# Performance work log

Measured on AMD Instinct MI355X. Metric: run time of the kernel, lower is better.

## Reference

```python
import jax, jax.numpy as jnp
import numpy as np

N_NODES = 100000
N_EDGES = 1600000
D = 128
L = 3


def setup_inputs() -> dict:
    key = jax.random.key(0)
    ks = jax.random.split(key, 5)
    x = jax.random.normal(ks[0], (N_NODES, D), dtype=jnp.float32)
    # Xavier-ish scale for stability through 3 layers
    scale = 1.0 / np.sqrt(D)
    W_self = jax.random.normal(ks[1], (L, D, D), dtype=jnp.float32) * scale
    W_neigh = jax.random.normal(ks[2], (L, D, D), dtype=jnp.float32) * scale
    bias = jnp.zeros((L, D), dtype=jnp.float32)
    src = jax.random.randint(ks[3], (N_EDGES,), 0, N_NODES)
    dst = jax.random.randint(ks[4], (N_EDGES,), 0, N_NODES)
    return {"x": x, "W_self": W_self, "W_neigh": W_neigh, "bias": bias,
            "src": src, "dst": dst}


def reference(x, W_self, W_neigh, bias, src, dst):
    """HomoSAGEEncoder forward (inference mode, dropout = identity).

    Each layer: DGL SAGEConv('mean'):
        h_neigh[v] = mean_{u in in-neighbors(v)} h[u]   (0 if no neighbors)
        h = h @ W_self + h_neigh @ W_neigh + bias
    followed by ReLU.
    """
    N = x.shape[0]
    n_layers = W_self.shape[0]
    # in-degree per destination node (shared across layers)
    deg = jax.ops.segment_sum(jnp.ones_like(dst, dtype=x.dtype), dst,
                              num_segments=N)
    inv_deg = (1.0 / jnp.maximum(deg, 1.0))[:, None]  # [N,1]

    h = x
    for l in range(n_layers):
        msg = h[src]  # [E,D] gather
        h_neigh = jax.ops.segment_sum(msg, dst, num_segments=N) * inv_deg
        h = h @ W_self[l] + h_neigh @ W_neigh[l] + bias[l]
        h = jax.nn.relu(h)
        # dropout is identity at inference; skipped
    return h
```

## Files before the change

kernel.cpp:

```cpp
#include <hip/hip_runtime.h>

typedef __attribute__((ext_vector_type(8))) short short8;
typedef __attribute__((ext_vector_type(4))) float f32x4;

static constexpr int NN = 100000;
static constexpr int NE = 1600000;
static constexpr int DD = 128;
static constexpr int NBUCK = 196;
static constexpr int CAP = 9216;

static constexpr int OFF_GCUR = 0;
static constexpr int OFF_OFFS = 512;
static constexpr int OFF_INV  = 100516;
static constexpr int OFF_WT   = 200520;
static constexpr int OFF_SS   = 249680;
static constexpr int OFF_HB   = 1849680;
static constexpr int OFF_HC   = 8249680;

__device__ inline ushort f2b(float f) {
  uint u = __builtin_bit_cast(uint, f);
  uint r = (u + 0x7fffu + ((u >> 16) & 1u)) >> 16;
  return (ushort)r;
}
__device__ inline float b2f(ushort b) {
  uint u = ((uint)b) << 16;
  return __builtin_bit_cast(float, u);
}

__global__ __launch_bounds__(256) void k_pre(const float* __restrict__ x,
                                             const float* __restrict__ Ws,
                                             const float* __restrict__ Wn,
                                             ushort* __restrict__ hb,
                                             ushort* __restrict__ WtP,
                                             int* __restrict__ gcur) {
  int b = blockIdx.x, t = threadIdx.x;
  if (b < 12500) {
    int i = b * 256 + t;
    float4 v = *(const float4*)(x + (size_t)i * 4);
    uint2 p;
    p.x = (uint)f2b(v.x) | ((uint)f2b(v.y) << 16);
    p.y = (uint)f2b(v.z) | ((uint)f2b(v.w) << 16);
    *(uint2*)(hb + (size_t)i * 4) = p;
  } else if (b < 12884) {
    int i = (b - 12500) * 256 + t;
    int j = i & 7;
    int kg = (i >> 3) & 3;
    int col = (i >> 5) & 127;
    int kt = (i >> 12) & 7;
    int l = i >> 15;
    int k = kt * 32 + kg * 8 + j;
    float v = (k < 128) ? Ws[((size_t)l * 128 + k) * 128 + col]
                        : Wn[((size_t)l * 128 + (k - 128)) * 128 + col];
    WtP[i] = f2b(v);
  } else {
    gcur[t] = 0;
  }
}

__global__ __launch_bounds__(256) void k_bucket(const int* __restrict__ src,
                                                const int* __restrict__ dst,
                                                int* __restrict__ gcur,
                                                int2* __restrict__ ebuf) {
  __shared__ int cnt[NBUCK], base[NBUCK];
  int t = threadIdx.x;
  int b0 = blockIdx.x * 4096;
  if (t < NBUCK) cnt[t] = 0;
  __syncthreads();
  int dv[16], pv[16];
#pragma unroll
  for (int j = 0; j < 16; ++j) {
    int idx = b0 + j * 256 + t;
    if (idx < NE) {
      int d = dst[idx];
      dv[j] = d;
      pv[j] = atomicAdd(&cnt[d >> 9], 1);
    } else dv[j] = -1;
  }
  __syncthreads();
  if (t < NBUCK) base[t] = atomicAdd(&gcur[t], cnt[t]);
  __syncthreads();
#pragma unroll
  for (int j = 0; j < 16; ++j) {
    if (dv[j] >= 0) {
      int idx = b0 + j * 256 + t;
      int b = dv[j] >> 9;
      int2 pr; pr.x = src[idx]; pr.y = dv[j];
      ebuf[(size_t)b * CAP + base[b] + pv[j]] = pr;
    }
  }
}

__global__ __launch_bounds__(256) void k_sort(const int2* __restrict__ ebuf,
                                              const int* __restrict__ gcur,
                                              int* __restrict__ offs,
                                              float* __restrict__ inv,
                                              int* __restrict__ ss) {
  __shared__ int cnt[512];
  __shared__ int sbase[512];
  __shared__ int scan[256];
  __shared__ int sarr[CAP];
  int b = blockIdx.x, t = threadIdx.x;
  int gv = (t < NBUCK) ? gcur[t] : 0;
  scan[t] = gv;
  __syncthreads();
  for (int off = 1; off < 256; off <<= 1) {
    int u = (t >= off) ? scan[t - off] : 0;
    __syncthreads();
    scan[t] += u;
    __syncthreads();
  }
  int nB = gcur[b];
  int base0 = scan[b] - nB;
  int n = nB;
  cnt[t] = 0; cnt[t + 256] = 0;
  __syncthreads();
  const int2* eb = ebuf + (size_t)b * CAP;
  for (int i = t; i < n; i += 256) atomicAdd(&cnt[eb[i].y & 511], 1);
  __syncthreads();
  int c0 = cnt[2 * t], c1 = cnt[2 * t + 1];
  int s = c0 + c1;
  scan[t] = s;
  __syncthreads();
  for (int off = 1; off < 256; off <<= 1) {
    int u = (t >= off) ? scan[t - off] : 0;
    __syncthreads();
    scan[t] += u;
    __syncthreads();
  }
  int eb2 = scan[t] - s;
  sbase[2 * t] = eb2;
  sbase[2 * t + 1] = eb2 + c0;
  int g0 = b * 512 + 2 * t, g1 = g0 + 1;
  if (g0 < NN) {
    offs[g0] = base0 + eb2;
    inv[g0] = 1.0f / (float)(c0 > 1 ? c0 : 1);
  }
  if (g1 < NN) {
    offs[g1] = base0 + eb2 + c0;
    inv[g1] = 1.0f / (float)(c1 > 1 ? c1 : 1);
  }
  if (b == NBUCK - 1 && t == 0) offs[NN] = NE;
  cnt[2 * t] = 0; cnt[2 * t + 1] = 0;
  __syncthreads();
  for (int i = t; i < n; i += 256) {
    int2 e = eb[i];
    int ln = e.y & 511;
    int p = sbase[ln] + atomicAdd(&cnt[ln], 1);
    sarr[p] = e.x;
  }
  __syncthreads();
  for (int i = t; i < n; i += 256) ss[base0 + i] = sarr[i];
}

__global__ __launch_bounds__(256) void k_fused(
    const ushort* __restrict__ hIn, const int* __restrict__ offs,
    const int* __restrict__ ss, const float* __restrict__ inv_deg,
    const ushort* __restrict__ WtP, const float* __restrict__ bias,
    ushort* __restrict__ hOut, float* __restrict__ outF, int writeF) {
  __shared__ ushort hN[128 * 128];
  int t = threadIdx.x;
  int w = t >> 6, lane = t & 63;
  int r = lane & 15, kg = lane >> 4;
  int row0 = blockIdx.x * 128;

  int colbase = w * 32;
  short8 bfrag[8][2];
#pragma unroll
  for (int kt = 0; kt < 8; ++kt)
#pragma unroll
    for (int nt = 0; nt < 2; ++nt) {
      int col = colbase + nt * 16 + r;
      bfrag[kt][nt] = *(const short8*)(WtP + ((size_t)(kt * 128 + col) * 4 + kg) * 8);
    }
  float bv[2];
  bv[0] = bias[colbase + r];
  bv[1] = bias[colbase + 16 + r];

  const ushort* hp = hIn + (size_t)r * 8;
#pragma unroll 1
  for (int g = 0; g < 8; ++g) {
    int lr = w * 32 + g * 4 + kg;
    int v = row0 + lr;
    float a0 = 0, a1 = 0, a2 = 0, a3 = 0, a4 = 0, a5 = 0, a6 = 0, a7 = 0;
    if (v < NN) {
      int beg = offs[v], end = offs[v + 1];
#define ACC8(u) { a0 += b2f((ushort)u.x); a1 += b2f((ushort)(u.x >> 16)); \
                  a2 += b2f((ushort)u.y); a3 += b2f((ushort)(u.y >> 16)); \
                  a4 += b2f((ushort)u.z); a5 += b2f((ushort)(u.z >> 16)); \
                  a6 += b2f((ushort)u.w); a7 += b2f((ushort)(u.w >> 16)); }
      int e = beg;
      for (; e + 7 < end; e += 8) {
        uint4 u0 = *(const uint4*)(hp + (size_t)ss[e + 0] * DD);
        uint4 u1 = *(const uint4*)(hp + (size_t)ss[e + 1] * DD);
        uint4 u2 = *(const uint4*)(hp + (size_t)ss[e + 2] * DD);
        uint4 u3 = *(const uint4*)(hp + (size_t)ss[e + 3] * DD);
        uint4 u4 = *(const uint4*)(hp + (size_t)ss[e + 4] * DD);
        uint4 u5 = *(const uint4*)(hp + (size_t)ss[e + 5] * DD);
        uint4 u6 = *(const uint4*)(hp + (size_t)ss[e + 6] * DD);
        uint4 u7 = *(const uint4*)(hp + (size_t)ss[e + 7] * DD);
        ACC8(u0) ACC8(u1) ACC8(u2) ACC8(u3) ACC8(u4) ACC8(u5) ACC8(u6) ACC8(u7)
      }
      for (; e < end; ++e) {
        uint4 u0 = *(const uint4*)(hp + (size_t)ss[e] * DD);
        ACC8(u0)
      }
#undef ACC8
      float sc = inv_deg[v];
      a0 *= sc; a1 *= sc; a2 *= sc; a3 *= sc;
      a4 *= sc; a5 *= sc; a6 *= sc; a7 *= sc;
    }
    uint4 p;
    p.x = (uint)f2b(a0) | ((uint)f2b(a1) << 16);
    p.y = (uint)f2b(a2) | ((uint)f2b(a3) << 16);
    p.z = (uint)f2b(a4) | ((uint)f2b(a5) << 16);
    p.w = (uint)f2b(a6) | ((uint)f2b(a7) << 16);
    *(uint4*)((char*)hN + lr * 256 + ((r * 16) ^ ((lr & 7) << 4))) = p;
  }
  __syncthreads();

  f32x4 acc[4][2][2];
#pragma unroll
  for (int it = 0; it < 4; ++it)
#pragma unroll
    for (int mt = 0; mt < 2; ++mt)
#pragma unroll
      for (int nt = 0; nt < 2; ++nt) acc[it][mt][nt] = (f32x4)0.f;

#pragma unroll
  for (int it = 0; it < 4; ++it) {
    int lr0 = it * 32 + r, lr1 = lr0 + 16;
    int ra0 = row0 + lr0; if (ra0 > NN - 1) ra0 = NN - 1;
    int ra1 = row0 + lr1; if (ra1 > NN - 1) ra1 = NN - 1;
#pragma unroll
    for (int kt = 0; kt < 8; ++kt) {
      short8 a0, a1;
      if (kt < 4) {
        int kk = kt * 32 + kg * 8;
        a0 = *(const short8*)(hIn + (size_t)ra0 * DD + kk);
        a1 = *(const short8*)(hIn + (size_t)ra1 * DD + kk);
      } else {
        int bo = (kt & 3) * 64 + kg * 16;
        a0 = *(const short8*)((char*)hN + lr0 * 256 + (bo ^ ((lr0 & 7) << 4)));
        a1 = *(const short8*)((char*)hN + lr1 * 256 + (bo ^ ((lr1 & 7) << 4)));
      }
      acc[it][0][0] = __builtin_amdgcn_mfma_f32_16x16x32_bf16(a0, bfrag[kt][0], acc[it][0][0], 0, 0, 0);
      acc[it][0][1] = __builtin_amdgcn_mfma_f32_16x16x32_bf16(a0, bfrag[kt][1], acc[it][0][1], 0, 0, 0);
      acc[it][1][0] = __builtin_amdgcn_mfma_f32_16x16x32_bf16(a1, bfrag[kt][0], acc[it][1][0], 0, 0, 0);
      acc[it][1][1] = __builtin_amdgcn_mfma_f32_16x16x32_bf16(a1, bfrag[kt][1], acc[it][1][1], 0, 0, 0);
    }
  }

#pragma unroll
  for (int it = 0; it < 4; ++it)
#pragma unroll
    for (int mt = 0; mt < 2; ++mt)
#pragma unroll
      for (int j = 0; j < 4; ++j) {
        int row = row0 + it * 32 + mt * 16 + kg * 4 + j;
        if (row < NN) {
#pragma unroll
          for (int nt = 0; nt < 2; ++nt) {
            float val = fmaxf(acc[it][mt][nt][j] + bv[nt], 0.f);
            int col = colbase + nt * 16 + r;
            if (writeF) outF[(size_t)row * DD + col] = val;
            else        hOut[(size_t)row * DD + col] = f2b(val);
          }
        }
      }
}

extern "C" void kernel_launch(void* const* d_in, const int* in_sizes, int n_in,
                              void* d_out, int out_size, void* d_ws, size_t ws_size,
                              hipStream_t stream) {
  const float* x    = (const float*)d_in[0];
  const float* Ws   = (const float*)d_in[1];
  const float* Wn   = (const float*)d_in[2];
  const float* bias = (const float*)d_in[3];
  const int*   src  = (const int*)d_in[4];
  const int*   dst  = (const int*)d_in[5];
  float* out = (float*)d_out;

  int* ws      = (int*)d_ws;
  int* gcur    = ws + OFF_GCUR;
  int* offs    = ws + OFF_OFFS;
  float* inv   = (float*)(ws + OFF_INV);
  ushort* WtP  = (ushort*)(ws + OFF_WT);
  int* ssorted = ws + OFF_SS;
  ushort* hB   = (ushort*)(ws + OFF_HB);
  ushort* hC   = (ushort*)(ws + OFF_HC);
  int2* ebuf   = (int2*)(ws + OFF_HC);

  k_pre<<<12885, 256, 0, stream>>>(x, Ws, Wn, hB, WtP, gcur);
  k_bucket<<<(NE + 4095) / 4096, 256, 0, stream>>>(src, dst, gcur, ebuf);
  k_sort<<<NBUCK, 256, 0, stream>>>(ebuf, gcur, offs, inv, ssorted);

  const ushort* hcur = hB;
  ushort* hnext = hC;
  for (int l = 0; l < 3; ++l) {
    k_fused<<<(NN + 127) / 128, 256, 0, stream>>>(
        hcur, offs, ssorted, inv, WtP + (size_t)l * 8 * 128 * 32,
        bias + l * DD, hnext, out, l == 2 ? 1 : 0);
    const ushort* tmp = hnext;
    hnext = (ushort*)hcur;
    hcur = tmp;
  }
}
```

Before: 569.8 us.

## Split fused aggregate+GEMM layer kernel into separate gather and GEMM kernels

Each layer's single fused kernel is replaced by two kernels. The first is a standalone neighbor-mean gather kernel, with each wave handling 4 nodes across many small blocks. The second is a 32-row-tile MFMA GEMM that reads the self and neighbor features from global memory and writes its output in place into the same hidden buffer, guarded by a block barrier. The aim is to remove the latency-bound serial gather loop and the large LDS tile that limited occupancy in the fused kernel. The cost is an extra global write and read of the bf16 neighbor matrix and an extra launch per layer.

Result: faster. 521.0 us (-8.6%).

```diff
diff --git a/kernel.cpp b/kernel.cpp
--- a/kernel.cpp
+++ b/kernel.cpp
@@ -15,7 +15,7 @@
 static constexpr int OFF_WT   = 200520;
 static constexpr int OFF_SS   = 249680;
 static constexpr int OFF_HB   = 1849680;
-static constexpr int OFF_HC   = 8249680;
+static constexpr int OFF_HNB  = 8249680;
 
 __device__ inline ushort f2b(float f) {
   uint u = __builtin_bit_cast(uint, f);
@@ -152,18 +152,60 @@
   for (int i = t; i < n; i += 256) ss[base0 + i] = sarr[i];
 }
 
-__global__ __launch_bounds__(256) void k_fused(
-    const ushort* __restrict__ hIn, const int* __restrict__ offs,
-    const int* __restrict__ ss, const float* __restrict__ inv_deg,
+__global__ __launch_bounds__(256) void k_agg3(const ushort* __restrict__ h,
+                                              const int* __restrict__ offs,
+                                              const int* __restrict__ ss,
+                                              const float* __restrict__ inv_deg,
+                                              ushort* __restrict__ hN) {
+  int gid = blockIdx.x * blockDim.x + threadIdx.x;
+  int wid = gid >> 6;
+  int lane = threadIdx.x & 63;
+  int q = lane >> 4, l16 = lane & 15;
+  int v = wid * 4 + q;
+  int beg = offs[v], end = offs[v + 1];
+  float a0 = 0, a1 = 0, a2 = 0, a3 = 0, a4 = 0, a5 = 0, a6 = 0, a7 = 0;
+  const ushort* hp = h + (size_t)l16 * 8;
+#define ACC8(u) { a0 += b2f((ushort)u.x); a1 += b2f((ushort)(u.x >> 16)); \
+                  a2 += b2f((ushort)u.y); a3 += b2f((ushort)(u.y >> 16)); \
+                  a4 += b2f((ushort)u.z); a5 += b2f((ushort)(u.z >> 16)); \
+                  a6 += b2f((ushort)u.w); a7 += b2f((ushort)(u.w >> 16)); }
+  int e = beg;
+  for (; e + 7 < end; e += 8) {
+    uint4 u0 = *(const uint4*)(hp + (size_t)ss[e + 0] * DD);
+    uint4 u1 = *(const uint4*)(hp + (size_t)ss[e + 1] * DD);
+    uint4 u2 = *(const uint4*)(hp + (size_t)ss[e + 2] * DD);
+    uint4 u3 = *(const uint4*)(hp + (size_t)ss[e + 3] * DD);
+    uint4 u4 = *(const uint4*)(hp + (size_t)ss[e + 4] * DD);
+    uint4 u5 = *(const uint4*)(hp + (size_t)ss[e + 5] * DD);
+    uint4 u6 = *(const uint4*)(hp + (size_t)ss[e + 6] * DD);
+    uint4 u7 = *(const uint4*)(hp + (size_t)ss[e + 7] * DD);
+    ACC8(u0) ACC8(u1) ACC8(u2) ACC8(u3) ACC8(u4) ACC8(u5) ACC8(u6) ACC8(u7)
+  }
+  for (; e < end; ++e) {
+    uint4 u0 = *(const uint4*)(hp + (size_t)ss[e] * DD);
+    ACC8(u0)
+  }
+#undef ACC8
+  float w = inv_deg[v];
+  a0 *= w; a1 *= w; a2 *= w; a3 *= w; a4 *= w; a5 *= w; a6 *= w; a7 *= w;
+  uint4 p;
+  p.x = (uint)f2b(a0) | ((uint)f2b(a1) << 16);
+  p.y = (uint)f2b(a2) | ((uint)f2b(a3) << 16);
+  p.z = (uint)f2b(a4) | ((uint)f2b(a5) << 16);
+  p.w = (uint)f2b(a6) | ((uint)f2b(a7) << 16);
+  *(uint4*)(hN + (size_t)v * DD + l16 * 8) = p;
+}
+
+__global__ __launch_bounds__(256) void k_gemm3(
+    const ushort* __restrict__ hA, const ushort* __restrict__ hNb,
     const ushort* __restrict__ WtP, const float* __restrict__ bias,
-    ushort* __restrict__ hOut, float* __restrict__ outF, int writeF) {
-  __shared__ ushort hN[128 * 128];
-  int t = threadIdx.x;
-  int w = t >> 6, lane = t & 63;
+    ushort* __restrict__ hOutB, float* __restrict__ outF, int writeF) {
+  int w = threadIdx.x >> 6;
+  int lane = threadIdx.x & 63;
   int r = lane & 15, kg = lane >> 4;
-  int row0 = blockIdx.x * 128;
-
   int colbase = w * 32;
+  int row0 = blockIdx.x * 32;
+
   short8 bfrag[8][2];
 #pragma unroll
   for (int kt = 0; kt < 8; ++kt)
@@ -176,97 +218,43 @@
   bv[0] = bias[colbase + r];
   bv[1] = bias[colbase + 16 + r];
 
-  const ushort* hp = hIn + (size_t)r * 8;
-#pragma unroll 1
-  for (int g = 0; g < 8; ++g) {
-    int lr = w * 32 + g * 4 + kg;
-    int v = row0 + lr;
-    float a0 = 0, a1 = 0, a2 = 0, a3 = 0, a4 = 0, a5 = 0, a6 = 0, a7 = 0;
-    if (v < NN) {
-      int beg = offs[v], end = offs[v + 1];
-#define ACC8(u) { a0 += b2f((ushort)u.x); a1 += b2f((ushort)(u.x >> 16)); \
-                  a2 += b2f((ushort)u.y); a3 += b2f((ushort)(u.y >> 16)); \
-                  a4 += b2f((ushort)u.z); a5 += b2f((ushort)(u.z >> 16)); \
-                  a6 += b2f((ushort)u.w); a7 += b2f((ushort)(u.w >> 16)); }
-      int e = beg;
-      for (; e + 7 < end; e += 8) {
-        uint4 u0 = *(const uint4*)(hp + (size_t)ss[e + 0] * DD);
-        uint4 u1 = *(const uint4*)(hp + (size_t)ss[e + 1] * DD);
-        uint4 u2 = *(const uint4*)(hp + (size_t)ss[e + 2] * DD);
-        uint4 u3 = *(const uint4*)(hp + (size_t)ss[e + 3] * DD);
-        uint4 u4 = *(const uint4*)(hp + (size_t)ss[e + 4] * DD);
-        uint4 u5 = *(const uint4*)(hp + (size_t)ss[e + 5] * DD);
-        uint4 u6 = *(const uint4*)(hp + (size_t)ss[e + 6] * DD);
-        uint4 u7 = *(const uint4*)(hp + (size_t)ss[e + 7] * DD);
-        ACC8(u0) ACC8(u1) ACC8(u2) ACC8(u3) ACC8(u4) ACC8(u5) ACC8(u6) ACC8(u7)
+  int ra0 = row0 + r;
+  int ra1 = row0 + 16 + r;
+
+  f32x4 acc[2][2];
+#pragma unroll
+  for (int mt = 0; mt < 2; ++mt)
+#pragma unroll
+    for (int nt = 0; nt < 2; ++nt) acc[mt][nt] = (f32x4)0.f;
+
+#pragma unroll
+  for (int kt = 0; kt < 8; ++kt) {
+    const ushort* hs = (kt < 4) ? hA : hNb;
+    int kk = (kt & 3) * 32 + kg * 8;
+    short8 a0 = *(const short8*)(hs + (size_t)ra0 * DD + kk);
+    short8 a1 = *(const short8*)(hs + (size_t)ra1 * DD + kk);
+    acc[0][0] = __builtin_amdgcn_mfma_f32_16x16x32_bf16(a0, bfrag[kt][0], acc[0][0], 0, 0, 0);
+    acc[0][1] = __builtin_amdgcn_mfma_f32_16x16x32_bf16(a0, bfrag[kt][1], acc[0][1], 0, 0, 0);
+    acc[1][0] = __builtin_amdgcn_mfma_f32_16x16x32_bf16(a1, bfrag[kt][0], acc[1][0], 0, 0, 0);
+    acc[1][1] = __builtin_amdgcn_mfma_f32_16x16x32_bf16(a1, bfrag[kt][1], acc[1][1], 0, 0, 0);
+  }
+
+  __syncthreads();
+
+#pragma unroll
+  for (int mt = 0; mt < 2; ++mt) {
+#pragma unroll
+    for (int j = 0; j < 4; ++j) {
+      int row = row0 + mt * 16 + kg * 4 + j;
+#pragma unroll
+      for (int nt = 0; nt < 2; ++nt) {
+        float val = fmaxf(acc[mt][nt][j] + bv[nt], 0.f);
+        int col = colbase + nt * 16 + r;
+        if (writeF) outF[(size_t)row * DD + col] = val;
+        else        hOutB[(size_t)row * DD + col] = f2b(val);
       }
-      for (; e < end; ++e) {
-        uint4 u0 = *(const uint4*)(hp + (size_t)ss[e] * DD);
-        ACC8(u0)
-      }
-#undef ACC8
-      float sc = inv_deg[v];
-      a0 *= sc; a1 *= sc; a2 *= sc; a3 *= sc;
-      a4 *= sc; a5 *= sc; a6 *= sc; a7 *= sc;
     }
-    uint4 p;
-    p.x = (uint)f2b(a0) | ((uint)f2b(a1) << 16);
-    p.y = (uint)f2b(a2) | ((uint)f2b(a3) << 16);
-    p.z = (uint)f2b(a4) | ((uint)f2b(a5) << 16);
-    p.w = (uint)f2b(a6) | ((uint)f2b(a7) << 16);
-    *(uint4*)((char*)hN + lr * 256 + ((r * 16) ^ ((lr & 7) << 4))) = p;
-  }
-  __syncthreads();
-
-  f32x4 acc[4][2][2];
-#pragma unroll
-  for (int it = 0; it < 4; ++it)
-#pragma unroll
-    for (int mt = 0; mt < 2; ++mt)
-#pragma unroll
-      for (int nt = 0; nt < 2; ++nt) acc[it][mt][nt] = (f32x4)0.f;
-
-#pragma unroll
-  for (int it = 0; it < 4; ++it) {
-    int lr0 = it * 32 + r, lr1 = lr0 + 16;
-    int ra0 = row0 + lr0; if (ra0 > NN - 1) ra0 = NN - 1;
-    int ra1 = row0 + lr1; if (ra1 > NN - 1) ra1 = NN - 1;
-#pragma unroll
-    for (int kt = 0; kt < 8; ++kt) {
-      short8 a0, a1;
-      if (kt < 4) {
-        int kk = kt * 32 + kg * 8;
-        a0 = *(const short8*)(hIn + (size_t)ra0 * DD + kk);
-        a1 = *(const short8*)(hIn + (size_t)ra1 * DD + kk);
-      } else {
-        int bo = (kt & 3) * 64 + kg * 16;
-        a0 = *(const short8*)((char*)hN + lr0 * 256 + (bo ^ ((lr0 & 7) << 4)));
-        a1 = *(const short8*)((char*)hN + lr1 * 256 + (bo ^ ((lr1 & 7) << 4)));
-      }
-      acc[it][0][0] = __builtin_amdgcn_mfma_f32_16x16x32_bf16(a0, bfrag[kt][0], acc[it][0][0], 0, 0, 0);
-      acc[it][0][1] = __builtin_amdgcn_mfma_f32_16x16x32_bf16(a0, bfrag[kt][1], acc[it][0][1], 0, 0, 0);
-      acc[it][1][0] = __builtin_amdgcn_mfma_f32_16x16x32_bf16(a1, bfrag[kt][0], acc[it][1][0], 0, 0, 0);
-      acc[it][1][1] = __builtin_amdgcn_mfma_f32_16x16x32_bf16(a1, bfrag[kt][1], acc[it][1][1], 0, 0, 0);
-    }
-  }
-
-#pragma unroll
-  for (int it = 0; it < 4; ++it)
-#pragma unroll
-    for (int mt = 0; mt < 2; ++mt)
-#pragma unroll
-      for (int j = 0; j < 4; ++j) {
-        int row = row0 + it * 32 + mt * 16 + kg * 4 + j;
-        if (row < NN) {
-#pragma unroll
-          for (int nt = 0; nt < 2; ++nt) {
-            float val = fmaxf(acc[it][mt][nt][j] + bv[nt], 0.f);
-            int col = colbase + nt * 16 + r;
-            if (writeF) outF[(size_t)row * DD + col] = val;
-            else        hOut[(size_t)row * DD + col] = f2b(val);
-          }
-        }
-      }
+  }
 }
 
 extern "C" void kernel_launch(void* const* d_in, const int* in_sizes, int n_in,
@@ -287,21 +275,16 @@
   ushort* WtP  = (ushort*)(ws + OFF_WT);
   int* ssorted = ws + OFF_SS;
   ushort* hB   = (ushort*)(ws + OFF_HB);
-  ushort* hC   = (ushort*)(ws + OFF_HC);
-  int2* ebuf   = (int2*)(ws + OFF_HC);
+  ushort* hNb  = (ushort*)(ws + OFF_HNB);
+  int2* ebuf   = (int2*)(ws + OFF_HNB);
 
   k_pre<<<12885, 256, 0, stream>>>(x, Ws, Wn, hB, WtP, gcur);
   k_bucket<<<(NE + 4095) / 4096, 256, 0, stream>>>(src, dst, gcur, ebuf);
   k_sort<<<NBUCK, 256, 0, stream>>>(ebuf, gcur, offs, inv, ssorted);
 
-  const ushort* hcur = hB;
-  ushort* hnext = hC;
   for (int l = 0; l < 3; ++l) {
-    k_fused<<<(NN + 127) / 128, 256, 0, stream>>>(
-        hcur, offs, ssorted, inv, WtP + (size_t)l * 8 * 128 * 32,
-        bias + l * DD, hnext, out, l == 2 ? 1 : 0);
-    const ushort* tmp = hnext;
-    hnext = (ushort*)hcur;
-    hcur = tmp;
-  }
-}
+    k_agg3<<<NN / 16, 256, 0, stream>>>(hB, offs, ssorted, inv, hNb);
+    k_gemm3<<<NN / 32, 256, 0, stream>>>(
+        hB, hNb, WtP + (size_t)l * 8 * 128 * 32, bias + l * DD, hB, out, l == 2 ? 1 : 0);
+  }
+}
```
